# Kernel optimization log

Measured on AMD Instinct MI355X. Metric: run time of the kernel, lower is better.

Reference implementation:

```python
import jax, jax.numpy as jnp
import numpy as np

B, E, H, F, L, A = 256, 1024, 1024, 2048, 196, 512
C_RATIO, H_RATIO = 0.5, 0.5


def setup_inputs() -> dict:
    key = jax.random.key(0)
    ks = jax.random.split(key, 20)
    u = lambda k, shape: jax.random.uniform(k, shape, jnp.float32, -0.1, 0.1)
    return {
        "xt": jax.random.normal(ks[0], (B, E), jnp.float32),
        "att_seq": jax.random.normal(ks[1], (B, L, F), jnp.float32),
        "h": jax.random.normal(ks[2], (B, H), jnp.float32),
        "c": jax.random.normal(ks[3], (B, H), jnp.float32),
        "Wi": u(ks[4], (4 * H, E)), "bi": u(ks[5], (4 * H,)),
        "Wh": u(ks[6], (4 * H, H)), "bh": u(ks[7], (4 * H,)),
        "Wz": u(ks[8], (4 * H, F)), "bz": u(ks[9], (4 * H,)),
        "Wa": u(ks[10], (A, F)), "ba": u(ks[11], (A,)),
        "Wha": u(ks[12], (A, H)), "bha": u(ks[13], (A,)),
        "Wo": u(ks[14], (1, A)), "bo": u(ks[15], (1,)),
    }


def reference(xt, att_seq, h, c, Wi, bi, Wh, bh, Wz, bz, Wa, ba, Wha, bha, Wo, bo):
    # attention scoring: tanh(att_2_att_h(att) + h_2_att_h(h)) -> scalar per location
    att_linear = jnp.einsum("blf,af->bla", att_seq, Wa) + ba          # [B,L,A]
    h_linear = h @ Wha.T + bha                                        # [B,A]
    att_h = jnp.tanh(att_linear + h_linear[:, None, :])               # [B,L,A]
    scores = jnp.einsum("bla,a->bl", att_h, Wo[0]) + bo[0]            # [B,L]
    w = jax.nn.softmax(scores, axis=-1)                               # [B,L]
    z = jnp.einsum("bl,blf->bf", w, att_seq)                          # [B,F] context

    # fused LSTM gates
    sums = (xt @ Wi.T + bi) + (h @ Wh.T + bh) + (z @ Wz.T + bz)       # [B,4H]
    i_g = jax.nn.sigmoid(sums[:, 0 * H:1 * H])
    f_g = jax.nn.sigmoid(sums[:, 1 * H:2 * H])
    o_g = jax.nn.sigmoid(sums[:, 2 * H:3 * H])
    g = jnp.tanh(sums[:, 3 * H:4 * H])

    # zoneout blending (training mode; dropout prob is 0 -> identity)
    next_c = c * C_RATIO + (1.0 - C_RATIO) * (f_g * c + i_g * g)
    next_h = h * H_RATIO + (1.0 - H_RATIO) * (o_g * jnp.tanh(next_c))
    return next_h, next_h, next_c  # (output, state_h, state_c)
```

## Files before the change

### kernel.cpp

```cpp
#include <hip/hip_runtime.h>

#define B_ 256
#define E_ 1024
#define H_ 1024
#define F_ 2048
#define L_ 196
#define A_ 512
#define ML (B_ * L_)

typedef __attribute__((ext_vector_type(8))) short short8;
typedef __attribute__((ext_vector_type(4))) float f32x4;

__device__ __forceinline__ unsigned short f2bf(float x) {
  unsigned u = __float_as_uint(x);
  unsigned r = (u + 0x7FFFu + ((u >> 16) & 1u)) >> 16;
  return (unsigned short)r;
}
__device__ __forceinline__ float bf2f(unsigned short u) {
  return __uint_as_float((unsigned)u << 16);
}
__device__ __forceinline__ float fast_tanh(float x) {
  x = fminf(fmaxf(x, -15.f), 15.f);
  float e = __expf(2.f * x);
  return (e - 1.f) / (e + 1.f);
}
__device__ __forceinline__ float sigmoidf_(float x) {
  return 1.f / (1.f + __expf(-x));
}

#define GLOAD_LDS(gptr, lptr) \
  __builtin_amdgcn_global_load_lds( \
      (const __attribute__((address_space(1))) void*)(gptr), \
      (__attribute__((address_space(3))) void*)(lptr), 16, 0, 0)

#define SBAR() asm volatile("s_barrier" ::: "memory")

__global__ void cast_wx_k(const float* __restrict__ Wa, const float* __restrict__ Wha,
                          const float* __restrict__ Wi, const float* __restrict__ Wh,
                          const float* __restrict__ Wz, const float* __restrict__ xt,
                          const float* __restrict__ h,
                          unsigned short* __restrict__ WaB, unsigned short* __restrict__ WhaB,
                          unsigned short* __restrict__ WgB, unsigned short* __restrict__ AgB) {
  size_t i = ((size_t)blockIdx.x * 256 + threadIdx.x) * 8;
  const float* src;
  unsigned short* dst;
  if (i < 1048576) { src = Wa + i; dst = WaB + i; }
  else if (i < 1572864) { src = Wha + (i - 1048576); dst = WhaB + (i - 1048576); }
  else if (i < 18350080) {
    size_t off = i - 1572864;
    int row = (int)(off >> 12), col = (int)(off & 4095);
    if (col < 1024)       src = Wi + (size_t)row * 1024 + col;
    else if (col < 2048)  src = Wh + (size_t)row * 1024 + (col - 1024);
    else                  src = Wz + (size_t)row * 2048 + (col - 2048);
    dst = WgB + off;
  } else {
    size_t off = i - 18350080;
    int row = (int)(off >> 11), col = (int)(off & 2047);
    src = (col < 1024) ? (xt + (size_t)row * 1024 + col) : (h + (size_t)row * 1024 + (col - 1024));
    dst = AgB + (size_t)row * 4096 + col;
  }
  float4 a = *reinterpret_cast<const float4*>(src);
  float4 b = *reinterpret_cast<const float4*>(src + 4);
  short8 o;
  o[0] = (short)f2bf(a.x); o[1] = (short)f2bf(a.y); o[2] = (short)f2bf(a.z); o[3] = (short)f2bf(a.w);
  o[4] = (short)f2bf(b.x); o[5] = (short)f2bf(b.y); o[6] = (short)f2bf(b.z); o[7] = (short)f2bf(b.w);
  *reinterpret_cast<short8*>(dst) = o;
}

__global__ __launch_bounds__(256, 2)
void hlin_gemm_k(const unsigned short* __restrict__ AgB, const unsigned short* __restrict__ WhaB,
                 const float* __restrict__ bha, float* __restrict__ hlin) {
  __shared__ unsigned short As[2][64 * 64];
  __shared__ unsigned short Bs[2][128 * 64];
  const int tid = threadIdx.x;
  const int lane = tid & 63, wid = tid >> 6;
  const int wm = wid >> 1, wn = wid & 1;
  const int m0 = blockIdx.y * 64;
  const int n0 = blockIdx.x * 128;
  const int g16 = lane >> 4, l16 = lane & 15;
  const int l7 = l16 & 7;
  f32x4 acc[2][4] = {};

#define STAGE_HL(BUF, KK)                                                                      \
  {                                                                                            \
    _Pragma("unroll")                                                                          \
    for (int it = 0; it < 2; ++it) {                                                           \
      int idx = it * 256 + tid;                                                                \
      int row = idx >> 3;                                                                      \
      int kc = (idx & 7) ^ (row & 7);                                                          \
      GLOAD_LDS(AgB + (size_t)(m0 + row) * 4096 + 1024 + (KK) + kc * 8, &As[BUF][idx * 8]);    \
    }                                                                                          \
    _Pragma("unroll")                                                                          \
    for (int it = 0; it < 4; ++it) {                                                           \
      int idx = it * 256 + tid;                                                                \
      int row = idx >> 3;                                                                      \
      int kc = (idx & 7) ^ (row & 7);                                                          \
      GLOAD_LDS(WhaB + (size_t)(n0 + row) * 1024 + (KK) + kc * 8, &Bs[BUF][idx * 8]);          \
    }                                                                                          \
  }

  STAGE_HL(0, 0);
  STAGE_HL(1, 64);
  asm volatile("s_waitcnt vmcnt(6)" ::: "memory");
  SBAR();
  int cur = 0;
  for (int k0 = 0; k0 < 1024; k0 += 64) {
    #pragma unroll
    for (int ks = 0; ks < 2; ++ks) {
      const int ko = ((ks * 4 + g16) ^ l7) << 3;
      short8 af[2], bfr[4];
      #pragma unroll
      for (int mi = 0; mi < 2; ++mi)
        af[mi] = *reinterpret_cast<const short8*>(&As[cur][(wm * 32 + mi * 16 + l16) * 64 + ko]);
      #pragma unroll
      for (int ni = 0; ni < 4; ++ni)
        bfr[ni] = *reinterpret_cast<const short8*>(&Bs[cur][(wn * 64 + ni * 16 + l16) * 64 + ko]);
      #pragma unroll
      for (int mi = 0; mi < 2; ++mi)
        #pragma unroll
        for (int ni = 0; ni < 4; ++ni)
          acc[mi][ni] = __builtin_amdgcn_mfma_f32_16x16x32_bf16(af[mi], bfr[ni], acc[mi][ni], 0, 0, 0);
    }
    SBAR();
    if (k0 + 128 < 1024) {
      STAGE_HL(cur, k0 + 128);
      asm volatile("s_waitcnt vmcnt(6)" ::: "memory");
    } else {
      asm volatile("s_waitcnt vmcnt(0)" ::: "memory");
    }
    SBAR();
    cur ^= 1;
  }
#undef STAGE_HL

  #pragma unroll
  for (int ni = 0; ni < 4; ++ni) {
    int col = n0 + wn * 64 + ni * 16 + l16;
    float bv = bha[col];
    #pragma unroll
    for (int mi = 0; mi < 2; ++mi)
      #pragma unroll
      for (int j = 0; j < 4; ++j) {
        int m = m0 + wm * 32 + mi * 16 + g16 * 4 + j;
        hlin[(size_t)m * A_ + col] = acc[mi][ni][j] + bv;
      }
  }
}

__global__ __launch_bounds__(256, 2)
void score_fuse_k(const float* __restrict__ att, const unsigned short* __restrict__ WaB,
                  const float* __restrict__ hlin, const float* __restrict__ ba,
                  const float* __restrict__ Wo, float* __restrict__ scores8) {
  __shared__ unsigned short As[2][128 * 64];
  __shared__ unsigned short Bs[2][128 * 64];
  const int tid = threadIdx.x;
  const int lane = tid & 63, wid = tid >> 6;
  const int wm = wid >> 1, wn = wid & 1;
  const int logical = (blockIdx.x & 7) * 196 + (blockIdx.x >> 3);
  const int m0 = (logical >> 2) * 128;
  const int n0 = (logical & 3) * 128;
  const int g16 = lane >> 4, l16 = lane & 15;
  const int l7 = l16 & 7;
  f32x4 acc[4][4] = {};
  float4 Ra[8], Rb[8];

#define LOADA(REG, KK)                                                                   \
  {                                                                                      \
    _Pragma("unroll")                                                                    \
    for (int it = 0; it < 8; ++it) {                                                     \
      int idx = it * 256 + tid;                                                          \
      int row = idx >> 4, kf = idx & 15;                                                 \
      REG[it] = *reinterpret_cast<const float4*>(att + (size_t)(m0 + row) * F_ + (KK) + kf * 4); \
    }                                                                                    \
  }
#define GLDB(BUF, KK)                                                                    \
  {                                                                                      \
    _Pragma("unroll")                                                                    \
    for (int it = 0; it < 4; ++it) {                                                     \
      int idx = it * 256 + tid;                                                          \
      int row = idx >> 3;                                                                \
      int kc = (idx & 7) ^ (row & 7);                                                    \
      GLOAD_LDS(WaB + (size_t)(n0 + row) * F_ + (KK) + kc * 8, &Bs[BUF][idx * 8]);       \
    }                                                                                    \
  }
#define WRITEA(BUF, REG)                                                                 \
  {                                                                                      \
    _Pragma("unroll")                                                                    \
    for (int it = 0; it < 8; ++it) {                                                     \
      int idx = it * 256 + tid;                                                          \
      int row = idx >> 4, kf = idx & 15;                                                 \
      float4 v = REG[it];                                                                \
      ushort4 o;                                                                         \
      o.x = f2bf(v.x); o.y = f2bf(v.y); o.z = f2bf(v.z); o.w = f2bf(v.w);                \
      int el = row * 64 + (((kf >> 1) ^ (row & 7)) << 3) + ((kf & 1) << 2);              \
      *reinterpret_cast<ushort4*>(&As[BUF][el]) = o;                                     \
    }                                                                                    \
  }
#define COMPUTE(BUF)                                                                     \
  {                                                                                      \
    _Pragma("unroll")                                                                    \
    for (int ks = 0; ks < 2; ++ks) {                                                     \
      const int ko = ((ks * 4 + g16) ^ l7) << 3;                                         \
      short8 af[4], bfr[4];                                                              \
      _Pragma("unroll")                                                                  \
      for (int mi = 0; mi < 4; ++mi)                                                     \
        af[mi] = *reinterpret_cast<const short8*>(&As[BUF][(wm * 64 + mi * 16 + l16) * 64 + ko]); \
      _Pragma("unroll")                                                                  \
      for (int ni = 0; ni < 4; ++ni)                                                     \
        bfr[ni] = *reinterpret_cast<const short8*>(&Bs[BUF][(wn * 64 + ni * 16 + l16) * 64 + ko]); \
      _Pragma("unroll")                                                                  \
      for (int mi = 0; mi < 4; ++mi)                                                     \
        _Pragma("unroll")                                                                \
        for (int ni = 0; ni < 4; ++ni)                                                   \
          acc[mi][ni] = __builtin_amdgcn_mfma_f32_16x16x32_bf16(af[mi], bfr[ni], acc[mi][ni], 0, 0, 0); \
    }                                                                                    \
  }

  LOADA(Ra, 0);  GLDB(0, 0);
  LOADA(Rb, 64); GLDB(1, 64);
  asm volatile("s_waitcnt vmcnt(12)" ::: "memory");
  WRITEA(0, Ra);
  asm volatile("s_waitcnt lgkmcnt(0)" ::: "memory");
  SBAR();

  for (int p = 0; p < 16; ++p) {
    const int t = 2 * p;
    COMPUTE(0);
    SBAR();
    if (t + 2 < 32) {
      LOADA(Ra, (t + 2) * 64); GLDB(0, (t + 2) * 64);
      asm volatile("s_waitcnt vmcnt(12)" ::: "memory");
    } else {
      asm volatile("s_waitcnt vmcnt(0)" ::: "memory");
    }
    WRITEA(1, Rb);
    asm volatile("s_waitcnt lgkmcnt(0)" ::: "memory");
    SBAR();
    COMPUTE(1);
    SBAR();
    if (t + 3 < 32) {
      LOADA(Rb, (t + 3) * 64); GLDB(1, (t + 3) * 64);
      asm volatile("s_waitcnt vmcnt(12)" ::: "memory");
    } else {
      asm volatile("s_waitcnt vmcnt(0)" ::: "memory");
    }
    if (t + 2 < 32) {
      WRITEA(0, Ra);
    }
    asm volatile("s_waitcnt lgkmcnt(0)" ::: "memory");
    SBAR();
  }
#undef LOADA
#undef GLDB
#undef WRITEA
#undef COMPUTE

  float wo_v[4], ba_v[4];
  int a_v[4];
  #pragma unroll
  for (int ni = 0; ni < 4; ++ni) {
    int a = n0 + wn * 64 + ni * 16 + l16;
    a_v[ni] = a; wo_v[ni] = Wo[a]; ba_v[ni] = ba[a];
  }
  const int slot = (n0 >> 7) * 2 + wn;
  #pragma unroll
  for (int mi = 0; mi < 4; ++mi) {
    float rs[4];
    #pragma unroll
    for (int j = 0; j < 4; ++j) {
      int m = m0 + wm * 64 + mi * 16 + g16 * 4 + j;
      int b = m / L_;
      const float* hb = hlin + (size_t)b * A_;
      float s = 0.f;
      #pragma unroll
      for (int ni = 0; ni < 4; ++ni) {
        float v = acc[mi][ni][j] + ba_v[ni] + hb[a_v[ni]];
        s += fast_tanh(v) * wo_v[ni];
      }
      rs[j] = s;
    }
    #pragma unroll
    for (int off = 1; off < 16; off <<= 1) {
      #pragma unroll
      for (int j = 0; j < 4; ++j) rs[j] += __shfl_xor(rs[j], off);
    }
    if (l16 == 0) {
      #pragma unroll
      for (int j = 0; j < 4; ++j) {
        int m = m0 + wm * 64 + mi * 16 + g16 * 4 + j;
        scores8[(size_t)m * 8 + slot] = rs[j];
      }
    }
  }
}

__global__ __launch_bounds__(256)
void z_sm_f32_k(const float* __restrict__ att, const float* __restrict__ scores8,
                unsigned short* __restrict__ AgB) {
  __shared__ float sm[L_];
  const int b = blockIdx.y;
  const int tid = threadIdx.x;
  if (tid < L_) {
    const float* p = scores8 + ((size_t)b * L_ + tid) * 8;
    float4 p0 = *reinterpret_cast<const float4*>(p);
    float4 p1 = *reinterpret_cast<const float4*>(p + 4);
    sm[tid] = (p0.x + p0.y) + (p0.z + p0.w) + (p1.x + p1.y) + (p1.z + p1.w);
  }
  __syncthreads();
  float mx = -1e30f;
  for (int l = 0; l < L_; ++l) mx = fmaxf(mx, sm[l]);
  float s = 0.f;
  for (int l = 0; l < L_; ++l) s += __expf(sm[l] - mx);
  const float inv = 1.f / s;
  __syncthreads();
  if (tid < L_) sm[tid] = __expf(sm[tid] - mx) * inv;
  __syncthreads();
  const int f0 = blockIdx.x * 1024 + tid * 4;
  const float* base = att + (size_t)b * L_ * F_ + f0;
  float a0 = 0.f, a1 = 0.f, a2 = 0.f, a3 = 0.f;
  #pragma unroll 4
  for (int l = 0; l < L_; ++l) {
    float wl = sm[l];
    float4 a = *reinterpret_cast<const float4*>(base + (size_t)l * F_);
    a0 += wl * a.x; a1 += wl * a.y; a2 += wl * a.z; a3 += wl * a.w;
  }
  ushort4 o;
  o.x = f2bf(a0); o.y = f2bf(a1); o.z = f2bf(a2); o.w = f2bf(a3);
  *reinterpret_cast<ushort4*>(AgB + (size_t)b * 4096 + 2048 + f0) = o;
}

__global__ __launch_bounds__(256, 4)
void gates_gemm_k(const unsigned short* __restrict__ AgB, const unsigned short* __restrict__ WgB,
                  const float* __restrict__ bi, const float* __restrict__ bh,
                  const float* __restrict__ bz, float* __restrict__ sums) {
  __shared__ unsigned short As[2][64 * 64];
  __shared__ unsigned short Bs[2][64 * 64];
  const int tid = threadIdx.x;
  const int lane = tid & 63, wid = tid >> 6;
  const int wm = wid >> 1, wn = wid & 1;
  const int m0 = blockIdx.y * 64;
  const int n0 = blockIdx.x * 64;
  const int g16 = lane >> 4, l16 = lane & 15;
  const int l7 = l16 & 7;
  f32x4 acc[2][2] = {};

#define STAGE_GG(BUF, KK)                                                               \
  {                                                                                     \
    _Pragma("unroll")                                                                   \
    for (int it = 0; it < 2; ++it) {                                                    \
      int idx = it * 256 + tid;                                                         \
      int row = idx >> 3;                                                               \
      int kc = (idx & 7) ^ (row & 7);                                                   \
      GLOAD_LDS(AgB + (size_t)(m0 + row) * 4096 + (KK) + kc * 8, &As[BUF][idx * 8]);    \
      GLOAD_LDS(WgB + (size_t)(n0 + row) * 4096 + (KK) + kc * 8, &Bs[BUF][idx * 8]);    \
    }                                                                                   \
  }

  STAGE_GG(0, 0);
  STAGE_GG(1, 64);
  asm volatile("s_waitcnt vmcnt(4)" ::: "memory");
  SBAR();
  int cur = 0;
  for (int k0 = 0; k0 < 4096; k0 += 64) {
    #pragma unroll
    for (int ks = 0; ks < 2; ++ks) {
      const int ko = ((ks * 4 + g16) ^ l7) << 3;
      short8 af[2], bfr[2];
      #pragma unroll
      for (int mi = 0; mi < 2; ++mi)
        af[mi] = *reinterpret_cast<const short8*>(&As[cur][(wm * 32 + mi * 16 + l16) * 64 + ko]);
      #pragma unroll
      for (int ni = 0; ni < 2; ++ni)
        bfr[ni] = *reinterpret_cast<const short8*>(&Bs[cur][(wn * 32 + ni * 16 + l16) * 64 + ko]);
      #pragma unroll
      for (int mi = 0; mi < 2; ++mi)
        #pragma unroll
        for (int ni = 0; ni < 2; ++ni)
          acc[mi][ni] = __builtin_amdgcn_mfma_f32_16x16x32_bf16(af[mi], bfr[ni], acc[mi][ni], 0, 0, 0);
    }
    SBAR();
    if (k0 + 128 < 4096) {
      STAGE_GG(cur, k0 + 128);
      asm volatile("s_waitcnt vmcnt(4)" ::: "memory");
    } else {
      asm volatile("s_waitcnt vmcnt(0)" ::: "memory");
    }
    SBAR();
    cur ^= 1;
  }
#undef STAGE_GG

  #pragma unroll
  for (int ni = 0; ni < 2; ++ni) {
    int col = n0 + wn * 32 + ni * 16 + l16;
    float bsum = bi[col] + bh[col] + bz[col];
    #pragma unroll
    for (int mi = 0; mi < 2; ++mi)
      #pragma unroll
      for (int j = 0; j < 4; ++j) {
        int m = m0 + wm * 32 + mi * 16 + g16 * 4 + j;
        sums[(size_t)m * 4096 + col] = acc[mi][ni][j] + bsum;
      }
  }
}

__global__ void final_k(const float* __restrict__ sums, const float* __restrict__ h,
                        const float* __restrict__ c, float* __restrict__ out) {
  int i = blockIdx.x * 256 + threadIdx.x;
  int b = i >> 10, hh = i & 1023;
  const float* srow = sums + (size_t)b * 4096;
  float ig = sigmoidf_(srow[hh]);
  float fg = sigmoidf_(srow[1024 + hh]);
  float og = sigmoidf_(srow[2048 + hh]);
  float g  = fast_tanh(srow[3072 + hh]);
  float cv = c[i], hv = h[i];
  float nc = 0.5f * cv + 0.5f * (fg * cv + ig * g);
  float nh = 0.5f * hv + 0.5f * (og * fast_tanh(nc));
  out[i] = nh;
  out[B_ * H_ + i] = nh;
  out[2 * B_ * H_ + i] = nc;
}

extern "C" void kernel_launch(void* const* d_in, const int* in_sizes, int n_in,
                              void* d_out, int out_size, void* d_ws, size_t ws_size,
                              hipStream_t stream) {
  const float* xt  = (const float*)d_in[0];
  const float* att = (const float*)d_in[1];
  const float* h   = (const float*)d_in[2];
  const float* c   = (const float*)d_in[3];
  const float* Wi  = (const float*)d_in[4];
  const float* bi  = (const float*)d_in[5];
  const float* Wh  = (const float*)d_in[6];
  const float* bh  = (const float*)d_in[7];
  const float* Wz  = (const float*)d_in[8];
  const float* bz  = (const float*)d_in[9];
  const float* Wa  = (const float*)d_in[10];
  const float* ba  = (const float*)d_in[11];
  const float* Wha = (const float*)d_in[12];
  const float* bha = (const float*)d_in[13];
  const float* Wo  = (const float*)d_in[14];

  char* ws = (char*)d_ws;
  const size_t MB = (size_t)1 << 20;
  unsigned short* WaB  = (unsigned short*)(ws);
  unsigned short* WhaB = (unsigned short*)(ws + 2 * MB);
  unsigned short* WgB  = (unsigned short*)(ws + 3 * MB);
  unsigned short* AgB  = (unsigned short*)(ws + 35 * MB);
  float* hlin    = (float*)(ws + 37 * MB);
  float* scores8 = (float*)(ws + 38 * MB);
  float* sums    = (float*)(ws + 40 * MB);
  float* out = (float*)d_out;

  cast_wx_k<<<9216, 256, 0, stream>>>(Wa, Wha, Wi, Wh, Wz, xt, h, WaB, WhaB, WgB, AgB);
  hlin_gemm_k<<<dim3(4, 4), 256, 0, stream>>>(AgB, WhaB, bha, hlin);
  score_fuse_k<<<(ML / 128) * (A_ / 128), 256, 0, stream>>>(att, WaB, hlin, ba, Wo, scores8);
  z_sm_f32_k<<<dim3(2, B_), 256, 0, stream>>>(att, scores8, AgB);
  gates_gemm_k<<<dim3(64, 4), 256, 0, stream>>>(AgB, WgB, bi, bh, bz, sums);
  final_k<<<B_ * H_ / 256, 256, 0, stream>>>(sums, h, c, out);
}
```

Baseline: 380.1 us.

## Load Wa fragments directly from global in score GEMM, drop B LDS staging

Measured after the change: 609.4 us. 60.3% more time.

```diff
diff --git a/kernel.cpp b/kernel.cpp
--- a/kernel.cpp
+++ b/kernel.cpp
@@ -15,9 +15,6 @@
   unsigned u = __float_as_uint(x);
   unsigned r = (u + 0x7FFFu + ((u >> 16) & 1u)) >> 16;
   return (unsigned short)r;
-}
-__device__ __forceinline__ float bf2f(unsigned short u) {
-  return __uint_as_float((unsigned)u << 16);
 }
 __device__ __forceinline__ float fast_tanh(float x) {
   x = fminf(fmaxf(x, -15.f), 15.f);
@@ -147,12 +144,11 @@
   }
 }
 
-__global__ __launch_bounds__(256, 2)
+__global__ __launch_bounds__(256, 3)
 void score_fuse_k(const float* __restrict__ att, const unsigned short* __restrict__ WaB,
                   const float* __restrict__ hlin, const float* __restrict__ ba,
                   const float* __restrict__ Wo, float* __restrict__ scores8) {
   __shared__ unsigned short As[2][128 * 64];
-  __shared__ unsigned short Bs[2][128 * 64];
   const int tid = threadIdx.x;
   const int lane = tid & 63, wid = tid >> 6;
   const int wm = wid >> 1, wn = wid & 1;
@@ -163,6 +159,10 @@
   const int l7 = l16 & 7;
   f32x4 acc[4][4] = {};
   float4 Ra[8], Rb[8];
+  const unsigned short* brow[4];
+  #pragma unroll
+  for (int ni = 0; ni < 4; ++ni)
+    brow[ni] = WaB + (size_t)(n0 + wn * 64 + ni * 16 + l16) * F_ + g16 * 8;
 
 #define LOADA(REG, KK)                                                                   \
   {                                                                                      \
@@ -173,16 +173,6 @@
       REG[it] = *reinterpret_cast<const float4*>(att + (size_t)(m0 + row) * F_ + (KK) + kf * 4); \
     }                                                                                    \
   }
-#define GLDB(BUF, KK)                                                                    \
-  {                                                                                      \
-    _Pragma("unroll")                                                                    \
-    for (int it = 0; it < 4; ++it) {                                                     \
-      int idx = it * 256 + tid;                                                          \
-      int row = idx >> 3;                                                                \
-      int kc = (idx & 7) ^ (row & 7);                                                    \
-      GLOAD_LDS(WaB + (size_t)(n0 + row) * F_ + (KK) + kc * 8, &Bs[BUF][idx * 8]);       \
-    }                                                                                    \
-  }
 #define WRITEA(BUF, REG)                                                                 \
   {                                                                                      \
     _Pragma("unroll")                                                                    \
@@ -190,24 +180,26 @@
       int idx = it * 256 + tid;                                                          \
       int row = idx >> 4, kf = idx & 15;                                                 \
       float4 v = REG[it];                                                                \
-      ushort4 o;                                                                         \
-      o.x = f2bf(v.x); o.y = f2bf(v.y); o.z = f2bf(v.z); o.w = f2bf(v.w);                \
+      unsigned lo, hi;                                                                   \
+      asm("v_cvt_pk_bf16_f32 %0, %1, %2" : "=v"(lo) : "v"(v.x), "v"(v.y));               \
+      asm("v_cvt_pk_bf16_f32 %0, %1, %2" : "=v"(hi) : "v"(v.z), "v"(v.w));               \
+      uint2 q; q.x = lo; q.y = hi;                                                       \
       int el = row * 64 + (((kf >> 1) ^ (row & 7)) << 3) + ((kf & 1) << 2);              \
-      *reinterpret_cast<ushort4*>(&As[BUF][el]) = o;                                     \
+      *reinterpret_cast<uint2*>(&As[BUF][el]) = q;                                       \
     }                                                                                    \
   }
-#define COMPUTE(BUF)                                                                     \
+#define COMPUTE(BUF, KK)                                                                 \
   {                                                                                      \
     _Pragma("unroll")                                                                    \
     for (int ks = 0; ks < 2; ++ks) {                                                     \
       const int ko = ((ks * 4 + g16) ^ l7) << 3;                                         \
       short8 af[4], bfr[4];                                                              \
       _Pragma("unroll")                                                                  \
+      for (int ni = 0; ni < 4; ++ni)                                                     \
+        bfr[ni] = *reinterpret_cast<const short8*>(brow[ni] + (KK) + ks * 32);           \
+      _Pragma("unroll")                                                                  \
       for (int mi = 0; mi < 4; ++mi)                                                     \
         af[mi] = *reinterpret_cast<const short8*>(&As[BUF][(wm * 64 + mi * 16 + l16) * 64 + ko]); \
-      _Pragma("unroll")                                                                  \
-      for (int ni = 0; ni < 4; ++ni)                                                     \
-        bfr[ni] = *reinterpret_cast<const short8*>(&Bs[BUF][(wn * 64 + ni * 16 + l16) * 64 + ko]); \
       _Pragma("unroll")                                                                  \
       for (int mi = 0; mi < 4; ++mi)                                                     \
         _Pragma("unroll")                                                                \
@@ -216,42 +208,35 @@
     }                                                                                    \
   }
 
-  LOADA(Ra, 0);  GLDB(0, 0);
-  LOADA(Rb, 64); GLDB(1, 64);
-  asm volatile("s_waitcnt vmcnt(12)" ::: "memory");
+  LOADA(Ra, 0);
+  LOADA(Rb, 64);
+  asm volatile("s_waitcnt vmcnt(8)" ::: "memory");
   WRITEA(0, Ra);
   asm volatile("s_waitcnt lgkmcnt(0)" ::: "memory");
   SBAR();
 
   for (int p = 0; p < 16; ++p) {
     const int t = 2 * p;
-    COMPUTE(0);
-    SBAR();
-    if (t + 2 < 32) {
-      LOADA(Ra, (t + 2) * 64); GLDB(0, (t + 2) * 64);
-      asm volatile("s_waitcnt vmcnt(12)" ::: "memory");
-    } else {
-      asm volatile("s_waitcnt vmcnt(0)" ::: "memory");
-    }
+    COMPUTE(0, t * 64);
+    if (t + 2 < 32) LOADA(Ra, (t + 2) * 64);
+    asm volatile("s_waitcnt vmcnt(16)" ::: "memory");
     WRITEA(1, Rb);
     asm volatile("s_waitcnt lgkmcnt(0)" ::: "memory");
     SBAR();
-    COMPUTE(1);
-    SBAR();
-    if (t + 3 < 32) {
-      LOADA(Rb, (t + 3) * 64); GLDB(1, (t + 3) * 64);
-      asm volatile("s_waitcnt vmcnt(12)" ::: "memory");
-    } else {
-      asm volatile("s_waitcnt vmcnt(0)" ::: "memory");
-    }
+    COMPUTE(1, (t + 1) * 64);
     if (t + 2 < 32) {
+      if (t + 3 < 32) {
+        LOADA(Rb, (t + 3) * 64);
+        asm volatile("s_waitcnt vmcnt(16)" ::: "memory");
+      } else {
+        asm volatile("s_waitcnt vmcnt(8)" ::: "memory");
+      }
       WRITEA(0, Ra);
     }
     asm volatile("s_waitcnt lgkmcnt(0)" ::: "memory");
     SBAR();
   }
 #undef LOADA
-#undef GLDB
 #undef WRITEA
 #undef COMPUTE
 
```

## Retile score GEMM to 64x256 blocks with single-buffered B and in-block score reduction

Applied to the files above, without the earlier changes.

After: 527.3 us. 1.39x slower.

```diff
diff --git a/kernel.cpp b/kernel.cpp
--- a/kernel.cpp
+++ b/kernel.cpp
@@ -16,9 +16,6 @@
   unsigned r = (u + 0x7FFFu + ((u >> 16) & 1u)) >> 16;
   return (unsigned short)r;
 }
-__device__ __forceinline__ float bf2f(unsigned short u) {
-  return __uint_as_float((unsigned)u << 16);
-}
 __device__ __forceinline__ float fast_tanh(float x) {
   x = fminf(fmaxf(x, -15.f), 15.f);
   float e = __expf(2.f * x);
@@ -34,6 +31,9 @@
       (__attribute__((address_space(3))) void*)(lptr), 16, 0, 0)
 
 #define SBAR() asm volatile("s_barrier" ::: "memory")
+#define LGKM0() asm volatile("s_waitcnt lgkmcnt(0)" ::: "memory")
+#define VMCNT(N) asm volatile("s_waitcnt vmcnt(" #N ")" ::: "memory")
+#define SCHEDB() __builtin_amdgcn_sched_barrier(0)
 
 __global__ void cast_wx_k(const float* __restrict__ Wa, const float* __restrict__ Wha,
                           const float* __restrict__ Wi, const float* __restrict__ Wh,
@@ -101,7 +101,7 @@
 
   STAGE_HL(0, 0);
   STAGE_HL(1, 64);
-  asm volatile("s_waitcnt vmcnt(6)" ::: "memory");
+  VMCNT(6);
   SBAR();
   int cur = 0;
   for (int k0 = 0; k0 < 1024; k0 += 64) {
@@ -121,12 +121,13 @@
         for (int ni = 0; ni < 4; ++ni)
           acc[mi][ni] = __builtin_amdgcn_mfma_f32_16x16x32_bf16(af[mi], bfr[ni], acc[mi][ni], 0, 0, 0);
     }
+    LGKM0();
     SBAR();
     if (k0 + 128 < 1024) {
       STAGE_HL(cur, k0 + 128);
-      asm volatile("s_waitcnt vmcnt(6)" ::: "memory");
+      VMCNT(6);
     } else {
-      asm volatile("s_waitcnt vmcnt(0)" ::: "memory");
+      VMCNT(0);
     }
     SBAR();
     cur ^= 1;
@@ -147,53 +148,54 @@
   }
 }
 
-__global__ __launch_bounds__(256, 2)
+__global__ __launch_bounds__(256, 3)
 void score_fuse_k(const float* __restrict__ att, const unsigned short* __restrict__ WaB,
                   const float* __restrict__ hlin, const float* __restrict__ ba,
-                  const float* __restrict__ Wo, float* __restrict__ scores8) {
-  __shared__ unsigned short As[2][128 * 64];
-  __shared__ unsigned short Bs[2][128 * 64];
+                  const float* __restrict__ Wo, float* __restrict__ scores2) {
+  __shared__ unsigned short As[2][64 * 64];
+  __shared__ unsigned short Bs[256 * 64];
   const int tid = threadIdx.x;
-  const int lane = tid & 63, wid = tid >> 6;
-  const int wm = wid >> 1, wn = wid & 1;
+  const int lane = tid & 63, wn = tid >> 6;
   const int logical = (blockIdx.x & 7) * 196 + (blockIdx.x >> 3);
-  const int m0 = (logical >> 2) * 128;
-  const int n0 = (logical & 3) * 128;
+  const int m0 = (logical >> 1) * 64;
+  const int n0 = (logical & 1) * 256;
   const int g16 = lane >> 4, l16 = lane & 15;
   const int l7 = l16 & 7;
   f32x4 acc[4][4] = {};
-  float4 Ra[8], Rb[8];
+  float4 Ra[4], Rb[4];
 
 #define LOADA(REG, KK)                                                                   \
+  {                                                                                      \
+    _Pragma("unroll")                                                                    \
+    for (int it = 0; it < 4; ++it) {                                                     \
+      int idx = it * 256 + tid;                                                          \
+      int row = idx >> 4, kf = idx & 15;                                                 \
+      REG[it] = *reinterpret_cast<const float4*>(att + (size_t)(m0 + row) * F_ + (KK) + kf * 4); \
+    }                                                                                    \
+  }
+#define GLDB(KK)                                                                         \
   {                                                                                      \
     _Pragma("unroll")                                                                    \
     for (int it = 0; it < 8; ++it) {                                                     \
       int idx = it * 256 + tid;                                                          \
-      int row = idx >> 4, kf = idx & 15;                                                 \
-      REG[it] = *reinterpret_cast<const float4*>(att + (size_t)(m0 + row) * F_ + (KK) + kf * 4); \
+      int row = idx >> 3;                                                                \
+      int kc = (idx & 7) ^ (row & 7);                                                    \
+      GLOAD_LDS(WaB + (size_t)(n0 + row) * F_ + (KK) + kc * 8, &Bs[idx * 8]);            \
     }                                                                                    \
   }
-#define GLDB(BUF, KK)                                                                    \
+#define WRITEA(BUF, REG)                                                                 \
   {                                                                                      \
     _Pragma("unroll")                                                                    \
     for (int it = 0; it < 4; ++it) {                                                     \
       int idx = it * 256 + tid;                                                          \
-      int row = idx >> 3;                                                                \
-      int kc = (idx & 7) ^ (row & 7);                                                    \
-      GLOAD_LDS(WaB + (size_t)(n0 + row) * F_ + (KK) + kc * 8, &Bs[BUF][idx * 8]);       \
-    }                                                                                    \
-  }
-#define WRITEA(BUF, REG)                                                                 \
-  {                                                                                      \
-    _Pragma("unroll")                                                                    \
-    for (int it = 0; it < 8; ++it) {                                                     \
-      int idx = it * 256 + tid;                                                          \
       int row = idx >> 4, kf = idx & 15;                                                 \
       float4 v = REG[it];                                                                \
-      ushort4 o;                                                                         \
-      o.x = f2bf(v.x); o.y = f2bf(v.y); o.z = f2bf(v.z); o.w = f2bf(v.w);                \
+      unsigned lo, hi;                                                                   \
+      asm("v_cvt_pk_bf16_f32 %0, %1, %2" : "=v"(lo) : "v"(v.x), "v"(v.y));               \
+      asm("v_cvt_pk_bf16_f32 %0, %1, %2" : "=v"(hi) : "v"(v.z), "v"(v.w));               \
+      uint2 q; q.x = lo; q.y = hi;                                                       \
       int el = row * 64 + (((kf >> 1) ^ (row & 7)) << 3) + ((kf & 1) << 2);              \
-      *reinterpret_cast<ushort4*>(&As[BUF][el]) = o;                                     \
+      *reinterpret_cast<uint2*>(&As[BUF][el]) = q;                                       \
     }                                                                                    \
   }
 #define COMPUTE(BUF)                                                                     \
@@ -204,10 +206,10 @@
       short8 af[4], bfr[4];                                                              \
       _Pragma("unroll")                                                                  \
       for (int mi = 0; mi < 4; ++mi)                                                     \
-        af[mi] = *reinterpret_cast<const short8*>(&As[BUF][(wm * 64 + mi * 16 + l16) * 64 + ko]); \
+        af[mi] = *reinterpret_cast<const short8*>(&As[BUF][(mi * 16 + l16) * 64 + ko]);  \
       _Pragma("unroll")                                                                  \
       for (int ni = 0; ni < 4; ++ni)                                                     \
-        bfr[ni] = *reinterpret_cast<const short8*>(&Bs[BUF][(wn * 64 + ni * 16 + l16) * 64 + ko]); \
+        bfr[ni] = *reinterpret_cast<const short8*>(&Bs[(wn * 64 + ni * 16 + l16) * 64 + ko]); \
       _Pragma("unroll")                                                                  \
       for (int mi = 0; mi < 4; ++mi)                                                     \
         _Pragma("unroll")                                                                \
@@ -216,45 +218,57 @@
     }                                                                                    \
   }
 
-  LOADA(Ra, 0);  GLDB(0, 0);
-  LOADA(Rb, 64); GLDB(1, 64);
-  asm volatile("s_waitcnt vmcnt(12)" ::: "memory");
+  LOADA(Ra, 0);
+  GLDB(0);
+  VMCNT(0);
   WRITEA(0, Ra);
-  asm volatile("s_waitcnt lgkmcnt(0)" ::: "memory");
+  LOADA(Rb, 64);
+  LGKM0();
   SBAR();
 
   for (int p = 0; p < 16; ++p) {
     const int t = 2 * p;
+    SCHEDB();
     COMPUTE(0);
-    SBAR();
+    LGKM0();
+    SBAR();
+    GLDB((t + 1) * 64);
+    VMCNT(8);
+    WRITEA(1, Rb);
     if (t + 2 < 32) {
-      LOADA(Ra, (t + 2) * 64); GLDB(0, (t + 2) * 64);
-      asm volatile("s_waitcnt vmcnt(12)" ::: "memory");
+      LOADA(Ra, (t + 2) * 64);
+      VMCNT(4);
     } else {
-      asm volatile("s_waitcnt vmcnt(0)" ::: "memory");
-    }
-    WRITEA(1, Rb);
-    asm volatile("s_waitcnt lgkmcnt(0)" ::: "memory");
-    SBAR();
+      VMCNT(0);
+    }
+    LGKM0();
+    SBAR();
+
+    SCHEDB();
     COMPUTE(1);
-    SBAR();
-    if (t + 3 < 32) {
-      LOADA(Rb, (t + 3) * 64); GLDB(1, (t + 3) * 64);
-      asm volatile("s_waitcnt vmcnt(12)" ::: "memory");
-    } else {
-      asm volatile("s_waitcnt vmcnt(0)" ::: "memory");
-    }
+    LGKM0();
+    SBAR();
     if (t + 2 < 32) {
+      GLDB((t + 2) * 64);
+      VMCNT(8);
       WRITEA(0, Ra);
-    }
-    asm volatile("s_waitcnt lgkmcnt(0)" ::: "memory");
-    SBAR();
+      if (t + 3 < 32) {
+        LOADA(Rb, (t + 3) * 64);
+        VMCNT(4);
+      } else {
+        VMCNT(0);
+      }
+      LGKM0();
+      SBAR();
+    }
   }
 #undef LOADA
 #undef GLDB
 #undef WRITEA
 #undef COMPUTE
 
+  __syncthreads();
+  float* red = (float*)&As[0][0];
   float wo_v[4], ba_v[4];
   int a_v[4];
   #pragma unroll
@@ -262,13 +276,12 @@
     int a = n0 + wn * 64 + ni * 16 + l16;
     a_v[ni] = a; wo_v[ni] = Wo[a]; ba_v[ni] = ba[a];
   }
-  const int slot = (n0 >> 7) * 2 + wn;
   #pragma unroll
   for (int mi = 0; mi < 4; ++mi) {
     float rs[4];
     #pragma unroll
     for (int j = 0; j < 4; ++j) {
-      int m = m0 + wm * 64 + mi * 16 + g16 * 4 + j;
+      int m = m0 + mi * 16 + g16 * 4 + j;
       int b = m / L_;
       const float* hb = hlin + (size_t)b * A_;
       float s = 0.f;
@@ -286,25 +299,26 @@
     }
     if (l16 == 0) {
       #pragma unroll
-      for (int j = 0; j < 4; ++j) {
-        int m = m0 + wm * 64 + mi * 16 + g16 * 4 + j;
-        scores8[(size_t)m * 8 + slot] = rs[j];
-      }
-    }
+      for (int j = 0; j < 4; ++j)
+        red[wn * 64 + mi * 16 + g16 * 4 + j] = rs[j];
+    }
+  }
+  __syncthreads();
+  if (tid < 64) {
+    float s = red[tid] + red[64 + tid] + red[128 + tid] + red[192 + tid];
+    scores2[(size_t)(m0 + tid) * 2 + (n0 >> 8)] = s;
   }
 }
 
 __global__ __launch_bounds__(256)
-void z_sm_f32_k(const float* __restrict__ att, const float* __restrict__ scores8,
+void z_sm_f32_k(const float* __restrict__ att, const float* __restrict__ scores2,
                 unsigned short* __restrict__ AgB) {
   __shared__ float sm[L_];
   const int b = blockIdx.y;
   const int tid = threadIdx.x;
   if (tid < L_) {
-    const float* p = scores8 + ((size_t)b * L_ + tid) * 8;
-    float4 p0 = *reinterpret_cast<const float4*>(p);
-    float4 p1 = *reinterpret_cast<const float4*>(p + 4);
-    sm[tid] = (p0.x + p0.y) + (p0.z + p0.w) + (p1.x + p1.y) + (p1.z + p1.w);
+    const float* p = scores2 + ((size_t)b * L_ + tid) * 2;
+    sm[tid] = p[0] + p[1];
   }
   __syncthreads();
   float mx = -1e30f;
@@ -358,7 +372,7 @@
 
   STAGE_GG(0, 0);
   STAGE_GG(1, 64);
-  asm volatile("s_waitcnt vmcnt(4)" ::: "memory");
+  VMCNT(4);
   SBAR();
   int cur = 0;
   for (int k0 = 0; k0 < 4096; k0 += 64) {
@@ -378,12 +392,13 @@
         for (int ni = 0; ni < 2; ++ni)
           acc[mi][ni] = __builtin_amdgcn_mfma_f32_16x16x32_bf16(af[mi], bfr[ni], acc[mi][ni], 0, 0, 0);
     }
+    LGKM0();
     SBAR();
     if (k0 + 128 < 4096) {
       STAGE_GG(cur, k0 + 128);
-      asm volatile("s_waitcnt vmcnt(4)" ::: "memory");
+      VMCNT(4);
     } else {
-      asm volatile("s_waitcnt vmcnt(0)" ::: "memory");
+      VMCNT(0);
     }
     SBAR();
     cur ^= 1;
@@ -447,14 +462,14 @@
   unsigned short* WgB  = (unsigned short*)(ws + 3 * MB);
   unsigned short* AgB  = (unsigned short*)(ws + 35 * MB);
   float* hlin    = (float*)(ws + 37 * MB);
-  float* scores8 = (float*)(ws + 38 * MB);
+  float* scores2 = (float*)(ws + 38 * MB);
   float* sums    = (float*)(ws + 40 * MB);
   float* out = (float*)d_out;
 
   cast_wx_k<<<9216, 256, 0, stream>>>(Wa, Wha, Wi, Wh, Wz, xt, h, WaB, WhaB, WgB, AgB);
   hlin_gemm_k<<<dim3(4, 4), 256, 0, stream>>>(AgB, WhaB, bha, hlin);
-  score_fuse_k<<<(ML / 128) * (A_ / 128), 256, 0, stream>>>(att, WaB, hlin, ba, Wo, scores8);
-  z_sm_f32_k<<<dim3(2, B_), 256, 0, stream>>>(att, scores8, AgB);
+  score_fuse_k<<<(ML / 64) * 2, 256, 0, stream>>>(att, WaB, hlin, ba, Wo, scores2);
+  z_sm_f32_k<<<dim3(2, B_), 256, 0, stream>>>(att, scores2, AgB);
   gates_gemm_k<<<dim3(64, 4), 256, 0, stream>>>(AgB, WgB, bi, bh, bz, sums);
   final_k<<<B_ * H_ / 256, 256, 0, stream>>>(sums, h, c, out);
 }
```
